# Kernel tuning notes

Hardware: AMD Instinct MI355X
Metric: run time of the kernel (lower is better)

Reference implementation:

```python
import jax, jax.numpy as jnp
import numpy as np

N = 50000      # num_nodes
NT = 300000    # unique (s, o) pairs
R = 64         # num relations
RP = 16        # latent pseudo-relations
E = 32         # emb_dim
C = 32         # num_classes
LW = 64        # latent MLP width


def setup_inputs() -> dict:
    key = jax.random.key(0)
    ks = jax.random.split(key, 12)
    inp = {
        "s_idx": jax.random.randint(ks[0], (NT,), 0, N, dtype=jnp.int32),
        "o_idx": jax.random.randint(ks[1], (NT,), 0, N, dtype=jnp.int32),
        "nhots": jax.random.uniform(ks[2], (NT, R), dtype=jnp.float32),
        "W1a": jax.random.normal(ks[3], (R, LW), dtype=jnp.float32) * 0.1,
        "b1a": jnp.zeros((LW,), jnp.float32),
        "W1b": jax.random.normal(ks[4], (LW, RP), dtype=jnp.float32) * 0.1,
        "b1b": jnp.zeros((RP,), jnp.float32),
        "W2a": jax.random.normal(ks[5], (R, LW), dtype=jnp.float32) * 0.1,
        "b2a": jnp.zeros((LW,), jnp.float32),
        "W2b": jax.random.normal(ks[6], (LW, RP), dtype=jnp.float32) * 0.1,
        "b2b": jnp.zeros((RP,), jnp.float32),
        "weights1": jax.random.normal(ks[7], (RP, N, E), dtype=jnp.float32) * 0.05,
        "weights2": jax.random.normal(ks[8], (RP, E, C), dtype=jnp.float32) * 0.05,
        "bias1": jnp.zeros((E,), jnp.float32),
        "bias2": jnp.zeros((C,), jnp.float32),
    }
    return inp


def _mlp(x, Wa, ba, Wb, bb):
    # Linear(r, lwidth) -> ReLU -> Linear(lwidth, rp)
    return jax.nn.relu(x @ Wa + ba) @ Wb + bb


def reference(s_idx, o_idx, nhots, W1a, b1a, W1b, b1b, W2a, b2a, W2b, b2b,
              weights1, weights2, bias1, bias2):
    n, rp = N, RP
    e = weights1.shape[2]
    k = jnp.arange(rp, dtype=s_idx.dtype)[:, None]   # [rp, 1]

    # hindices: rows = s (tiled k-major), cols = o * k  -> sparse (n, n*rp)
    hrows = jnp.tile(s_idx, rp)                       # [rp*nt]
    hcols = (o_idx[None, :] * k).reshape(-1)          # [rp*nt]
    # vindices: rows = s * k, cols = o (tiled)        -> sparse (n*rp, n)
    vrows = (s_idx[None, :] * k).reshape(-1)
    vcols = jnp.tile(o_idx, rp)

    # ---- layer 1: latent relation softmax + column-normalized spmm ----
    lat1 = jax.nn.softmax(_mlp(nhots, W1a, b1a, W1b, b1b), axis=1)  # [nt, rp]
    v1 = lat1.T.reshape(-1)                                          # [rp*nt], k-major
    colsum = jax.ops.segment_sum(v1, hcols, num_segments=n * rp)
    v1 = v1 / colsum[hcols]
    # spmm: out[s] += v1 * weights1.view(rp*n, e)[o*k]
    h = jax.ops.segment_sum(v1[:, None] * weights1.reshape(rp * n, e)[hcols],
                            hrows, num_segments=n)                   # [n, e]
    h = jax.nn.relu(h + bias1)

    # ---- layer 2: latent relation softmax + row-normalized spmm ----
    lat2 = jax.nn.softmax(_mlp(nhots, W2a, b2a, W2b, b2b), axis=1)   # [nt, rp]
    v2 = lat2.T.reshape(-1)
    rowsum = jax.ops.segment_sum(v2, vrows, num_segments=n * rp)
    v2 = v2 / rowsum[vrows]
    # spmm: out[s*k] += v2 * h[o]
    h2 = jax.ops.segment_sum(v2[:, None] * h[vcols],
                             vrows, num_segments=n * rp)             # [n*rp, e]
    h2 = h2.reshape(rp, n, e)

    out = jnp.einsum('rhc,rnh->nc', weights2, h2) + bias2            # [n, c]
    return out
```

## Files before the change

### kernel.cpp

```cpp
#include <hip/hip_runtime.h>
#include <hip/hip_bf16.h>

#define DEV_INLINE __device__ __forceinline__

constexpr int kN   = 50000;
constexpr int kNT  = 300000;
constexpr int kR   = 64;
constexpr int kRP  = 16;
constexpr int kE   = 32;
constexpr int kC   = 32;
constexpr int kLW  = 64;
constexpr int kNRP = kN * kRP;
constexpr int kChunks = (kN + 255) / 256;

typedef __attribute__((ext_vector_type(8))) short s8v;
typedef __attribute__((ext_vector_type(4))) float f32x4;

DEV_INLINE short f2bf(float f) {
  union { float f; unsigned u; } v; v.f = f;
  unsigned r = (v.u + 0x7fffu + ((v.u >> 16) & 1u)) >> 16;
  return (short)r;
}
DEV_INLINE float bf2f(short s) {
  union { unsigned u; float f; } v; v.u = ((unsigned)(unsigned short)s) << 16;
  return v.f;
}
DEV_INLINE float bflo(unsigned u) { union { unsigned x; float f; } a; a.x = u << 16;        return a.f; }
DEV_INLINE float bfhi(unsigned u) { union { unsigned x; float f; } a; a.x = u & 0xffff0000u; return a.f; }

union U4S8 { uint4 u; s8v s; };

DEV_INLINE void split8(const float4 A, const float4 B, s8v& hi, s8v& lo) {
  const float f[8] = {A.x, A.y, A.z, A.w, B.x, B.y, B.z, B.w};
  unsigned u[8], l[8];
#pragma unroll
  for (int i = 0; i < 8; i++) { union { float f; unsigned u; } c; c.f = f[i]; u[i] = c.u; }
#pragma unroll
  for (int i = 0; i < 8; i++) {
    union { unsigned u; float f; } t; t.u = u[i] & 0xffff0000u;
    union { float f; unsigned u; } c; c.f = f[i] - t.f; l[i] = c.u;
  }
  U4S8 H, L;
  H.u.x = (u[1] & 0xffff0000u) | (u[0] >> 16);
  H.u.y = (u[3] & 0xffff0000u) | (u[2] >> 16);
  H.u.z = (u[5] & 0xffff0000u) | (u[4] >> 16);
  H.u.w = (u[7] & 0xffff0000u) | (u[6] >> 16);
  L.u.x = (l[1] & 0xffff0000u) | (l[0] >> 16);
  L.u.y = (l[3] & 0xffff0000u) | (l[2] >> 16);
  L.u.z = (l[5] & 0xffff0000u) | (l[4] >> 16);
  L.u.w = (l[7] & 0xffff0000u) | (l[6] >> 16);
  hi = H.s; lo = L.s;
}

__global__ void __launch_bounds__(256)
k_count(const int* __restrict__ s_idx, const int* __restrict__ o_idx,
        int* __restrict__ cnt_s, int* __restrict__ cnt_o) {
  const int e = blockIdx.x * 256 + threadIdx.x;
  if (e < kNT) {
    atomicAdd(&cnt_s[s_idx[e]], 1);
    atomicAdd(&cnt_o[o_idx[e]], 1);
  }
}

__global__ void __launch_bounds__(256)
k_scan_p1(const int* __restrict__ cnt_s, const int* __restrict__ cnt_o,
          int* __restrict__ rp_s, int* __restrict__ rp_o,
          int* __restrict__ bs_s, int* __restrict__ bs_o) {
  const int b = blockIdx.x;
  const bool iso = b >= kChunks;
  const int chunk = iso ? b - kChunks : b;
  const int* cnt = iso ? cnt_o : cnt_s;
  int* rp = iso ? rp_o : rp_s;
  int* bs = iso ? bs_o : bs_s;
  __shared__ int ws[4];
  const int tid = threadIdx.x, wave = tid >> 6, lane = tid & 63;
  const int i = chunk * 256 + tid;
  int v = (i < kN) ? cnt[i] : 0;
  int incl = v;
#pragma unroll
  for (int off = 1; off < 64; off <<= 1) {
    int tmp = __shfl_up(incl, off, 64);
    if (lane >= off) incl += tmp;
  }
  if (lane == 63) ws[wave] = incl;
  __syncthreads();
  int add = 0;
#pragma unroll
  for (int w = 0; w < 4; w++) if (w < wave) add += ws[w];
  incl += add;
  if (i < kN) rp[i + 1] = incl;
  if (tid == 255) bs[chunk] = incl;
}

__global__ void __launch_bounds__(256)
k_scan_p2(int* __restrict__ bs_s, int* __restrict__ bs_o) {
  __shared__ int ws[4];
  const int tid = threadIdx.x, wave = tid >> 6, lane = tid & 63;
#pragma unroll 1
  for (int a = 0; a < 2; a++) {
    int* bs = a ? bs_o : bs_s;
    const int v = (tid < kChunks) ? bs[tid] : 0;
    int incl = v;
#pragma unroll
    for (int off = 1; off < 64; off <<= 1) {
      int tmp = __shfl_up(incl, off, 64);
      if (lane >= off) incl += tmp;
    }
    if (lane == 63) ws[wave] = incl;
    __syncthreads();
    int add = 0;
#pragma unroll
    for (int w = 0; w < 4; w++) if (w < wave) add += ws[w];
    incl += add;
    __syncthreads();
    if (tid < kChunks) bs[tid] = incl - v;
    __syncthreads();
  }
}

__global__ void __launch_bounds__(256)
k_scan_p3(const int* __restrict__ bs_s, const int* __restrict__ bs_o,
          int* __restrict__ rp_s, int* __restrict__ rp_o) {
  const int b = blockIdx.x;
  const bool iso = b >= kChunks;
  const int chunk = iso ? b - kChunks : b;
  int* rp = iso ? rp_o : rp_s;
  const int* bs = iso ? bs_o : bs_s;
  const int i = chunk * 256 + threadIdx.x;
  if (i < kN) rp[i + 1] += bs[chunk];
  if (chunk == 0 && threadIdx.x == 0) rp[0] = 0;
}

__global__ void __launch_bounds__(256)
k_scatter2(const int* __restrict__ s_idx, const int* __restrict__ o_idx,
           const int* __restrict__ rowptr_s, int* __restrict__ cursor_s,
           const int* __restrict__ rowptr_o, int* __restrict__ cursor_o,
           int2* __restrict__ eo_s, int* __restrict__ e_o) {
  const int e = blockIdx.x * 256 + threadIdx.x;
  if (e < kNT) {
    const int s = s_idx[e], o = o_idx[e];
    const int ps = atomicAdd(&cursor_s[s], 1);
    int2 v; v.x = e; v.y = o;
    eo_s[rowptr_s[s] + ps] = v;
    const int po = atomicAdd(&cursor_o[o], 1);
    e_o[rowptr_o[o] + po] = e;
  }
}

__global__ void __launch_bounds__(256)
k_wprep(const float* __restrict__ W1a, const float* __restrict__ W1b,
        const float* __restrict__ W2a, const float* __restrict__ W2b,
        short* __restrict__ Wf) {
  const int tid = threadIdx.x;
  for (int i = tid; i < 8192; i += 256) {
    const int j = i & 7, lane = (i >> 3) & 63, ks = (i >> 9) & 1,
              nt = (i >> 10) & 3, mlp = i >> 12;
    const int p = lane & 15, q8 = (lane >> 4) * 8;
    const float* Wa = mlp ? W2a : W1a;
    const float v = Wa[(ks * 32 + q8 + j) * kLW + nt * 16 + p];
    union { float f; unsigned u; } c; c.f = v;
    const short h = (short)(c.u >> 16);
    Wf[i] = h;
    Wf[8192 + i] = f2bf(v - bf2f(h));
  }
  for (int i = tid; i < 2048; i += 256) {
    const int j = i & 7, lane = (i >> 3) & 63, ks = (i >> 9) & 1, mlp = i >> 10;
    const int p = lane & 15, q8 = (lane >> 4) * 8;
    const float* Wb = mlp ? W2b : W1b;
    const float v = Wb[(ks * 32 + q8 + j) * kRP + p];
    union { float f; unsigned u; } c; c.f = v;
    const short h = (short)(c.u >> 16);
    Wf[16384 + i] = h;
    Wf[18432 + i] = f2bf(v - bf2f(h));
  }
}

__global__ void __launch_bounds__(256)
k_lat(const float* __restrict__ nhots, const short* __restrict__ Wf,
      const float* __restrict__ b1a, const float* __restrict__ b1b,
      const float* __restrict__ b2a, const float* __restrict__ b2b,
      const int* __restrict__ s_idx, const int* __restrict__ o_idx,
      float* __restrict__ lat1o, float* __restrict__ lat2o,
      float* __restrict__ C1, float* __restrict__ R2) {
  __shared__ float sHf[4][16][68];
  const int tid = threadIdx.x;
  const int wave = tid >> 6, lane = tid & 63;
  const int p = lane & 15, q = lane >> 4, q8 = (lane >> 4) * 8;

  const uint4* BaH4 = (const uint4*)(Wf);
  const uint4* BaL4 = (const uint4*)(Wf + 8192);
  const uint4* BbH4 = (const uint4*)(Wf + 16384);
  const uint4* BbL4 = (const uint4*)(Wf + 18432);

  const int w2 = (blockIdx.x * 4 + wave) * 2;

#pragma unroll 1
  for (int mlp = 0; mlp < 2; mlp++) {
    s8v Bh[4][2], Bl[4][2], Bbh[2], Bbl[2];
#pragma unroll
    for (int nt = 0; nt < 4; nt++)
#pragma unroll
      for (int ks = 0; ks < 2; ks++) {
        U4S8 a, b;
        a.u = BaH4[((mlp * 4 + nt) * 2 + ks) * 64 + lane];
        b.u = BaL4[((mlp * 4 + nt) * 2 + ks) * 64 + lane];
        Bh[nt][ks] = a.s; Bl[nt][ks] = b.s;
      }
#pragma unroll
    for (int ks = 0; ks < 2; ks++) {
      U4S8 a, b;
      a.u = BbH4[(mlp * 2 + ks) * 64 + lane];
      b.u = BbL4[(mlp * 2 + ks) * 64 + lane];
      Bbh[ks] = a.s; Bbl[ks] = b.s;
    }
    const float* bA = mlp ? b2a : b1a;
    const float* bB = mlp ? b2b : b1b;
    float bav[4];
#pragma unroll
    for (int nt = 0; nt < 4; nt++) bav[nt] = bA[nt * 16 + p];
    const float bbv = bB[p];
    float* lato = mlp ? lat2o : lat1o;
    const int* nidx = mlp ? s_idx : o_idx;
    float* part = mlp ? R2 : C1;

#pragma unroll 1
    for (int t = 0; t < 2; t++) {
      const int slot = w2 + t;
      if (slot >= kNT / 32) break;
      const int eb = slot * 32;
#pragma unroll 1
      for (int ht = 0; ht < 2; ht++) {
        const int mb = eb + ht * 16;
        int nid[4];
#pragma unroll
        for (int reg = 0; reg < 4; reg++) nid[reg] = nidx[mb + q * 4 + reg];
        const float* arow = nhots + (size_t)(mb + p) * kR;
        s8v ah[2], al[2];
#pragma unroll
        for (int ks = 0; ks < 2; ks++) {
          const float4 xa = *(const float4*)(arow + ks * 32 + q8);
          const float4 xb = *(const float4*)(arow + ks * 32 + q8 + 4);
          split8(xa, xb, ah[ks], al[ks]);
        }
        f32x4 acc[4];
#pragma unroll
        for (int nt = 0; nt < 4; nt++) {
          acc[nt] = (f32x4)0.f;
#pragma unroll
          for (int ks = 0; ks < 2; ks++) {
            acc[nt] = __builtin_amdgcn_mfma_f32_16x16x32_bf16(ah[ks], Bh[nt][ks], acc[nt], 0, 0, 0);
            acc[nt] = __builtin_amdgcn_mfma_f32_16x16x32_bf16(ah[ks], Bl[nt][ks], acc[nt], 0, 0, 0);
            acc[nt] = __builtin_amdgcn_mfma_f32_16x16x32_bf16(al[ks], Bh[nt][ks], acc[nt], 0, 0, 0);
          }
        }
#pragma unroll
        for (int nt = 0; nt < 4; nt++)
#pragma unroll
          for (int reg = 0; reg < 4; reg++)
            sHf[wave][q * 4 + reg][nt * 16 + p] = fmaxf(acc[nt][reg] + bav[nt], 0.f);
        const float* hr = &sHf[wave][p][0];
        s8v hh[2], hl[2];
#pragma unroll
        for (int ks = 0; ks < 2; ks++) {
          const float4 xa = *(const float4*)(hr + ks * 32 + q8);
          const float4 xb = *(const float4*)(hr + ks * 32 + q8 + 4);
          split8(xa, xb, hh[ks], hl[ks]);
        }
        f32x4 accB = (f32x4)0.f;
#pragma unroll
        for (int ks = 0; ks < 2; ks++) {
          accB = __builtin_amdgcn_mfma_f32_16x16x32_bf16(hh[ks], Bbh[ks], accB, 0, 0, 0);
          accB = __builtin_amdgcn_mfma_f32_16x16x32_bf16(hh[ks], Bbl[ks], accB, 0, 0, 0);
          accB = __builtin_amdgcn_mfma_f32_16x16x32_bf16(hl[ks], Bbh[ks], accB, 0, 0, 0);
        }
#pragma unroll
        for (int reg = 0; reg < 4; reg++) {
          const float v = accB[reg] + bbv;
          float m = v;
#pragma unroll
          for (int d = 1; d < 16; d <<= 1) m = fmaxf(m, __shfl_xor(m, d));
          const float e = __expf(v - m);
          float sum = e;
#pragma unroll
          for (int d = 1; d < 16; d <<= 1) sum += __shfl_xor(sum, d);
          const float lv = e / sum;
          lato[(size_t)(mb + q * 4 + reg) * kRP + p] = lv;
          atomicAdd(&part[(size_t)nid[reg] * kRP + p], lv);
        }
      }
    }
  }
}

__global__ void __launch_bounds__(256)
k_tots(const float* __restrict__ C1, const float* __restrict__ R2,
       float* __restrict__ tots) {
  __shared__ float s0[4], s1[4];
  const int tid = threadIdx.x, wave = tid >> 6, lane = tid & 63;
  float a = 0.f, b = 0.f;
  for (int i = blockIdx.x * 256 + tid; i < kN; i += gridDim.x * 256) {
    a += C1[(size_t)i * kRP];
    b += R2[(size_t)i * kRP];
  }
#pragma unroll
  for (int d = 1; d < 64; d <<= 1) { a += __shfl_xor(a, d); b += __shfl_xor(b, d); }
  if (lane == 0) { s0[wave] = a; s1[wave] = b; }
  __syncthreads();
  if (tid == 0) {
    atomicAdd(&tots[0], s0[0] + s0[1] + s0[2] + s0[3]);
    atomicAdd(&tots[1], s1[0] + s1[1] + s1[2] + s1[3]);
  }
}

__global__ void __launch_bounds__(256)
k_norms(const float* __restrict__ C1, const float* __restrict__ R2,
        const float* __restrict__ tots,
        float* __restrict__ csinv, float* __restrict__ rsinv) {
  const int m = blockIdx.x * 256 + threadIdx.x;
  if (m < kNRP) {
    float cs = (m == 0) ? tots[0] : 0.f;
    float rs = (m == 0) ? tots[1] : 0.f;
#pragma unroll
    for (int k = 1; k < kRP; k++) {
      if (m % k == 0) {
        const int q = m / k;
        if (q < kN) { cs += C1[q * kRP + k]; rs += R2[q * kRP + k]; }
      }
    }
    csinv[m] = (cs != 0.f) ? 1.f / cs : 0.f;
    rsinv[m] = (rs != 0.f) ? 1.f / rs : 0.f;
  }
}

__global__ void __launch_bounds__(256)
k_gbuild(const float* __restrict__ wt1, const float* __restrict__ csinv,
         unsigned* __restrict__ G8u) {
  __shared__ float sT[16][33];
  const int o = blockIdx.x;
  const int tid = threadIdx.x;
#pragma unroll
  for (int half = 0; half < 2; half++) {
    const int e = half * 256 + tid;
    const int k = e >> 5, c = e & 31;
    const int idx = o * k;
    sT[k][c] = csinv[idx] * wt1[(size_t)idx * kE + c];
  }
  __syncthreads();
  const int l = tid >> 2;
  const int c = l >> 1, kh = l & 1;
  const int j0 = (2 * tid) & 7;
  const int k0 = kh * 8 + j0, k1 = k0 + 1;
  const unsigned lo = (unsigned short)f2bf(sT[k0][c]);
  const unsigned hi = (unsigned short)f2bf(sT[k1][c]);
  G8u[(size_t)o * 256 + tid] = lo | (hi << 16);
}

__global__ void __launch_bounds__(256)
k_layer1g(const int* __restrict__ rowptr, const int2* __restrict__ eo,
          const float* __restrict__ lat1, const uint4* __restrict__ G8,
          const float* __restrict__ bias1, float* __restrict__ h) {
  const int tid = threadIdx.x;
  const int wave = tid >> 6, lane = tid & 63;
  const int c = lane >> 1, kh = lane & 1;
  const float b1 = bias1[c];
  for (int s = blockIdx.x * 4 + wave; s < kN; s += gridDim.x * 4) {
    float acc = 0.f;
    const int beg = rowptr[s], end = rowptr[s + 1];
    for (int j = beg; j < end; j++) {
      const int2 E = eo[j];
      const uint4 g = G8[(size_t)E.y * 64 + lane];
      const float4 la = *(const float4*)(lat1 + (size_t)E.x * kRP + kh * 8);
      const float4 lb = *(const float4*)(lat1 + (size_t)E.x * kRP + kh * 8 + 4);
      acc = fmaf(la.x, bflo(g.x), acc); acc = fmaf(la.y, bfhi(g.x), acc);
      acc = fmaf(la.z, bflo(g.y), acc); acc = fmaf(la.w, bfhi(g.y), acc);
      acc = fmaf(lb.x, bflo(g.z), acc); acc = fmaf(lb.y, bfhi(g.z), acc);
      acc = fmaf(lb.z, bflo(g.w), acc); acc = fmaf(lb.w, bfhi(g.w), acc);
    }
    acc += __shfl_xor(acc, 1);
    if (kh == 0) h[(size_t)s * kE + c] = fmaxf(acc + b1, 0.f);
  }
}

__global__ void __launch_bounds__(256)
k_u(const int* __restrict__ rowptr, const int2* __restrict__ eo,
    const float* __restrict__ lat2, const float* __restrict__ rsinv,
    const float* __restrict__ h, short* __restrict__ Ub,
    float* __restrict__ pblk) {
  __shared__ float sacc[kE];
  const int tid = threadIdx.x;
  const int wave = tid >> 6, lane = tid & 63;
  const int c = lane & 31, half = lane >> 5;
  if (tid < kE) sacc[tid] = 0.f;
  __syncthreads();
  float hpart = 0.f;
  for (int s = blockIdx.x * 4 + wave; s < kN; s += gridDim.x * 4) {
    float u[8];
#pragma unroll
    for (int kk = 0; kk < 8; kk++) u[kk] = 0.f;
    const int beg = rowptr[s], end = rowptr[s + 1];
    for (int j = beg; j < end; j++) {
      const int2 E = eo[j];
      const float hv = h[(size_t)E.y * kE + c];
      const float4* lp = (const float4*)(lat2 + (size_t)E.x * kRP) + half * 2;
      const float4 la = lp[0], lb = lp[1];
      const float lv[8] = {la.x, la.y, la.z, la.w, lb.x, lb.y, lb.z, lb.w};
#pragma unroll
      for (int kk = 0; kk < 8; kk++) u[kk] = fmaf(lv[kk], hv, u[kk]);
    }
    if (half == 0) hpart += u[0];
#pragma unroll
    for (int kk = 0; kk < 8; kk++) {
      const int k = half * 8 + kk;
      if (k >= 1)
        Ub[((size_t)s * 15 + (k - 1)) * kE + c] = f2bf(u[kk] * rsinv[s * k]);
    }
  }
  atomicAdd(&sacc[c], hpart);
  __syncthreads();
  if (tid < kE) pblk[(size_t)blockIdx.x * kE + tid] = sacc[tid];
}

__global__ void __launch_bounds__(256)
k_hred(const float* __restrict__ pblk, int nblk, float* __restrict__ hrow0) {
  __shared__ float sacc[kE];
  const int tid = threadIdx.x;
  if (tid < kE) sacc[tid] = 0.f;
  __syncthreads();
  const int total = nblk * kE;
  float r = 0.f;
  for (int i = blockIdx.x * 256 + tid; i < total; i += gridDim.x * 256)
    r += pblk[i];
  atomicAdd(&sacc[tid & 31], r);
  __syncthreads();
  if (tid < kE) atomicAdd(&hrow0[tid], sacc[tid]);
}

__global__ void __launch_bounds__(256)
k_h2(const short* __restrict__ Ub, const float* __restrict__ hrow0,
     const float* __restrict__ rsinv, short* __restrict__ H2) {
  const int tid = threadIdx.x;
  const int g = tid >> 5, c = tid & 31;
  const int n = blockIdx.x * 8 + g;
  const float rs0 = rsinv[0];
  int nm[16];
  nm[0] = 0; nm[1] = 0;
#pragma unroll
  for (int k = 2; k < kRP; k++) nm[k] = n % k;
#pragma unroll
  for (int r = 0; r < kRP; r++) {
    float row = 0.f;
    if (r == 0 && n == 0) row = hrow0[c] * rs0;
#pragma unroll
    for (int k = r + 1; k < kRP; k++) {
      const int target = (k - (r * 50000) % k) % k;
      if (nm[k] == target) {
        const int s = (r * 50000 + n) / k;
        row += bf2f(Ub[((size_t)s * 15 + (k - 1)) * kE + c]);
      }
    }
    H2[((size_t)n * kRP + r) * kE + c] = f2bf(row);
  }
}

__global__ void __launch_bounds__(256)
k_einsum(const short* __restrict__ H2, const float* __restrict__ W2,
         const float* __restrict__ bias2, float* __restrict__ out) {
  __shared__ short sBWh[16 * 2 * 64 * 8];
  __shared__ short sBWl[16 * 2 * 64 * 8];
  const int tid = threadIdx.x;
  for (int i = tid; i < 16384; i += 256) {
    const int j = i & 7, ln = (i >> 3) & 63, nt = (i >> 9) & 1, ks = i >> 10;
    const int pp = ln & 15, qq8 = (ln >> 4) * 8;
    const float v = W2[(ks * 32 + qq8 + j) * 32 + nt * 16 + pp];
    const short h = f2bf(v);
    sBWh[i] = h;
    sBWl[i] = f2bf(v - bf2f(h));
  }
  __syncthreads();
  const int wave = tid >> 6, lane = tid & 63;
  const int p = lane & 15, q = lane >> 4, q8 = q * 8;
  const float bias0 = bias2[p], bias1v = bias2[16 + p];
  for (int tile = blockIdx.x * 4 + wave; tile < kN / 16; tile += gridDim.x * 4) {
    const int mb = tile * 16;
    f32x4 acc0 = (f32x4)0.f, acc1 = (f32x4)0.f;
    const short* arow = H2 + (size_t)(mb + p) * 512 + q8;
#pragma unroll
    for (int ks = 0; ks < 16; ks++) {
      const s8v a   = *(const s8v*)(arow + ks * 32);
      const s8v b0h = *(const s8v*)(sBWh + ((ks * 2 + 0) * 64 + lane) * 8);
      const s8v b0l = *(const s8v*)(sBWl + ((ks * 2 + 0) * 64 + lane) * 8);
      const s8v b1h = *(const s8v*)(sBWh + ((ks * 2 + 1) * 64 + lane) * 8);
      const s8v b1l = *(const s8v*)(sBWl + ((ks * 2 + 1) * 64 + lane) * 8);
      acc0 = __builtin_amdgcn_mfma_f32_16x16x32_bf16(a, b0h, acc0, 0, 0, 0);
      acc0 = __builtin_amdgcn_mfma_f32_16x16x32_bf16(a, b0l, acc0, 0, 0, 0);
      acc1 = __builtin_amdgcn_mfma_f32_16x16x32_bf16(a, b1h, acc1, 0, 0, 0);
      acc1 = __builtin_amdgcn_mfma_f32_16x16x32_bf16(a, b1l, acc1, 0, 0, 0);
    }
#pragma unroll
    for (int reg = 0; reg < 4; reg++) {
      const int n = mb + q * 4 + reg;
      out[(size_t)n * kC + p]      = acc0[reg] + bias0;
      out[(size_t)n * kC + 16 + p] = acc1[reg] + bias1v;
    }
  }
}

extern "C" void kernel_launch(void* const* d_in, const int* in_sizes, int n_in,
                              void* d_out, int out_size, void* d_ws, size_t ws_size,
                              hipStream_t stream) {
  (void)in_sizes; (void)n_in; (void)out_size; (void)ws_size;
  const int* s_idx = (const int*)d_in[0];
  const int* o_idx = (const int*)d_in[1];
  const float* nhots = (const float*)d_in[2];
  const float* W1a = (const float*)d_in[3]; const float* b1a = (const float*)d_in[4];
  const float* W1b = (const float*)d_in[5]; const float* b1b = (const float*)d_in[6];
  const float* W2a = (const float*)d_in[7]; const float* b2a = (const float*)d_in[8];
  const float* W2b = (const float*)d_in[9]; const float* b2b = (const float*)d_in[10];
  const float* wt1 = (const float*)d_in[11]; const float* wt2 = (const float*)d_in[12];
  const float* bias1 = (const float*)d_in[13]; const float* bias2 = (const float*)d_in[14];

  char* ws = (char*)d_ws;
  size_t off = 0;
  auto alloc = [&](size_t bytes) -> char* {
    char* p = ws + off;
    off = (off + bytes + 255) & ~(size_t)255;
    return p;
  };
  char*  z0       = ws;
  int*   cnt_s    = (int*)  alloc((size_t)kN * 4);
  int*   cnt_o    = (int*)  alloc((size_t)kN * 4);
  int*   cursor_s = (int*)  alloc((size_t)kN * 4);
  int*   cursor_o = (int*)  alloc((size_t)kN * 4);
  float* tots     = (float*)alloc(8);
  float* hrow0    = (float*)alloc((size_t)kE * 4);
  float* C1       = (float*)alloc((size_t)kNRP * 4);
  float* R2       = (float*)alloc((size_t)kNRP * 4);
  const size_t zbytes = (size_t)((ws + off) - z0);
  short* Wf       = (short*)alloc((size_t)20480 * 2);
  int*   bs_s     = (int*)  alloc((size_t)kChunks * 4);
  int*   bs_o     = (int*)  alloc((size_t)kChunks * 4);
  int*   rowptr_s = (int*)  alloc((size_t)(kN + 1) * 4);
  int*   rowptr_o = (int*)  alloc((size_t)(kN + 1) * 4);
  float* pblk     = (float*)alloc((size_t)12500 * kE * 4);
  float* lat2     = (float*)alloc((size_t)kNT * kRP * 4);
  int2*  eo_s     = (int2*) alloc((size_t)kNT * 8);
  int*   e_o      = (int*)  alloc((size_t)kNT * 4);
  float* csinv    = (float*)alloc((size_t)kNRP * 4);
  float* rsinv    = (float*)alloc((size_t)kNRP * 4);
  float* hbuf     = (float*)alloc((size_t)kN * kE * 4);
  short* Ub       = (short*)alloc((size_t)kN * 15 * kE * 2);
  char*  Greg     = alloc((size_t)kN * 1024);
  float* lat1     = (float*)Ub;
  unsigned* G8u   = (unsigned*)Greg;
  short* H2       = (short*)Greg;

  hipMemsetAsync(z0, 0, zbytes, stream);

  const dim3 blk(256);
  const int gEdges = (kNT + 255) / 256;
  const int gLat = ((kNT / 32 + 1) / 2 + 3) / 4;

  k_count<<<gEdges, blk, 0, stream>>>(s_idx, o_idx, cnt_s, cnt_o);
  k_scan_p1<<<2 * kChunks, blk, 0, stream>>>(cnt_s, cnt_o, rowptr_s, rowptr_o, bs_s, bs_o);
  k_scan_p2<<<1, blk, 0, stream>>>(bs_s, bs_o);
  k_scan_p3<<<2 * kChunks, blk, 0, stream>>>(bs_s, bs_o, rowptr_s, rowptr_o);
  k_scatter2<<<gEdges, blk, 0, stream>>>(s_idx, o_idx, rowptr_s, cursor_s,
                                         rowptr_o, cursor_o, eo_s, e_o);
  k_wprep<<<1, blk, 0, stream>>>(W1a, W1b, W2a, W2b, Wf);
  k_lat<<<gLat, blk, 0, stream>>>(nhots, Wf, b1a, b1b, b2a, b2b,
                                  s_idx, o_idx, lat1, lat2, C1, R2);
  k_tots<<<64, blk, 0, stream>>>(C1, R2, tots);
  k_norms<<<(kNRP + 255) / 256, blk, 0, stream>>>(C1, R2, tots, csinv, rsinv);
  k_gbuild<<<kN, blk, 0, stream>>>(wt1, csinv, G8u);
  k_layer1g<<<12500, blk, 0, stream>>>(rowptr_s, eo_s, lat1, (const uint4*)G8u, bias1, hbuf);
  k_u<<<12500, blk, 0, stream>>>(rowptr_s, eo_s, lat2, rsinv, hbuf, Ub, pblk);
  k_hred<<<50, blk, 0, stream>>>(pblk, 12500, hrow0);
  k_h2<<<kN / 8, blk, 0, stream>>>(Ub, hrow0, rsinv, H2);
  k_einsum<<<782, blk, 0, stream>>>(H2, wt2, bias2, (float*)d_out);
}
```

Before: 586.3 us.

## Write latents in s-sorted CSR order, drop unused o-CSR, prefetch gather loads

```diff
diff --git a/kernel.cpp b/kernel.cpp
--- a/kernel.cpp
+++ b/kernel.cpp
@@ -53,28 +53,16 @@
 }
 
 __global__ void __launch_bounds__(256)
-k_count(const int* __restrict__ s_idx, const int* __restrict__ o_idx,
-        int* __restrict__ cnt_s, int* __restrict__ cnt_o) {
+k_count(const int* __restrict__ s_idx, int* __restrict__ cnt_s) {
   const int e = blockIdx.x * 256 + threadIdx.x;
-  if (e < kNT) {
-    atomicAdd(&cnt_s[s_idx[e]], 1);
-    atomicAdd(&cnt_o[o_idx[e]], 1);
-  }
-}
-
-__global__ void __launch_bounds__(256)
-k_scan_p1(const int* __restrict__ cnt_s, const int* __restrict__ cnt_o,
-          int* __restrict__ rp_s, int* __restrict__ rp_o,
-          int* __restrict__ bs_s, int* __restrict__ bs_o) {
-  const int b = blockIdx.x;
-  const bool iso = b >= kChunks;
-  const int chunk = iso ? b - kChunks : b;
-  const int* cnt = iso ? cnt_o : cnt_s;
-  int* rp = iso ? rp_o : rp_s;
-  int* bs = iso ? bs_o : bs_s;
+  if (e < kNT) atomicAdd(&cnt_s[s_idx[e]], 1);
+}
+
+__global__ void __launch_bounds__(256)
+k_scan_p1(const int* __restrict__ cnt, int* __restrict__ rp, int* __restrict__ bs) {
   __shared__ int ws[4];
   const int tid = threadIdx.x, wave = tid >> 6, lane = tid & 63;
-  const int i = chunk * 256 + tid;
+  const int i = blockIdx.x * 256 + tid;
   int v = (i < kN) ? cnt[i] : 0;
   int incl = v;
 #pragma unroll
@@ -89,61 +77,47 @@
   for (int w = 0; w < 4; w++) if (w < wave) add += ws[w];
   incl += add;
   if (i < kN) rp[i + 1] = incl;
-  if (tid == 255) bs[chunk] = incl;
-}
-
-__global__ void __launch_bounds__(256)
-k_scan_p2(int* __restrict__ bs_s, int* __restrict__ bs_o) {
+  if (tid == 255) bs[blockIdx.x] = incl;
+}
+
+__global__ void __launch_bounds__(256)
+k_scan_p2(int* __restrict__ bs) {
   __shared__ int ws[4];
   const int tid = threadIdx.x, wave = tid >> 6, lane = tid & 63;
-#pragma unroll 1
-  for (int a = 0; a < 2; a++) {
-    int* bs = a ? bs_o : bs_s;
-    const int v = (tid < kChunks) ? bs[tid] : 0;
-    int incl = v;
-#pragma unroll
-    for (int off = 1; off < 64; off <<= 1) {
-      int tmp = __shfl_up(incl, off, 64);
-      if (lane >= off) incl += tmp;
-    }
-    if (lane == 63) ws[wave] = incl;
-    __syncthreads();
-    int add = 0;
-#pragma unroll
-    for (int w = 0; w < 4; w++) if (w < wave) add += ws[w];
-    incl += add;
-    __syncthreads();
-    if (tid < kChunks) bs[tid] = incl - v;
-    __syncthreads();
-  }
-}
-
-__global__ void __launch_bounds__(256)
-k_scan_p3(const int* __restrict__ bs_s, const int* __restrict__ bs_o,
-          int* __restrict__ rp_s, int* __restrict__ rp_o) {
-  const int b = blockIdx.x;
-  const bool iso = b >= kChunks;
-  const int chunk = iso ? b - kChunks : b;
-  int* rp = iso ? rp_o : rp_s;
-  const int* bs = iso ? bs_o : bs_s;
-  const int i = chunk * 256 + threadIdx.x;
-  if (i < kN) rp[i + 1] += bs[chunk];
-  if (chunk == 0 && threadIdx.x == 0) rp[0] = 0;
-}
-
-__global__ void __launch_bounds__(256)
-k_scatter2(const int* __restrict__ s_idx, const int* __restrict__ o_idx,
-           const int* __restrict__ rowptr_s, int* __restrict__ cursor_s,
-           const int* __restrict__ rowptr_o, int* __restrict__ cursor_o,
-           int2* __restrict__ eo_s, int* __restrict__ e_o) {
+  const int v = (tid < kChunks) ? bs[tid] : 0;
+  int incl = v;
+#pragma unroll
+  for (int off = 1; off < 64; off <<= 1) {
+    int tmp = __shfl_up(incl, off, 64);
+    if (lane >= off) incl += tmp;
+  }
+  if (lane == 63) ws[wave] = incl;
+  __syncthreads();
+  int add = 0;
+#pragma unroll
+  for (int w = 0; w < 4; w++) if (w < wave) add += ws[w];
+  incl += add;
+  if (tid < kChunks) bs[tid] = incl - v;
+}
+
+__global__ void __launch_bounds__(256)
+k_scan_p3(const int* __restrict__ bs, int* __restrict__ rp) {
+  const int i = blockIdx.x * 256 + threadIdx.x;
+  if (i < kN) rp[i + 1] += bs[blockIdx.x];
+  if (blockIdx.x == 0 && threadIdx.x == 0) rp[0] = 0;
+}
+
+__global__ void __launch_bounds__(256)
+k_scatter(const int* __restrict__ s_idx, const int* __restrict__ o_idx,
+          const int* __restrict__ rowptr, int* __restrict__ cursor,
+          int* __restrict__ o_csr, int* __restrict__ sslot) {
   const int e = blockIdx.x * 256 + threadIdx.x;
   if (e < kNT) {
-    const int s = s_idx[e], o = o_idx[e];
-    const int ps = atomicAdd(&cursor_s[s], 1);
-    int2 v; v.x = e; v.y = o;
-    eo_s[rowptr_s[s] + ps] = v;
-    const int po = atomicAdd(&cursor_o[o], 1);
-    e_o[rowptr_o[o] + po] = e;
+    const int s = s_idx[e];
+    const int ps = atomicAdd(&cursor[s], 1);
+    const int slot = rowptr[s] + ps;
+    o_csr[slot] = o_idx[e];
+    sslot[e] = slot;
   }
 }
 
@@ -180,6 +154,7 @@
       const float* __restrict__ b1a, const float* __restrict__ b1b,
       const float* __restrict__ b2a, const float* __restrict__ b2b,
       const int* __restrict__ s_idx, const int* __restrict__ o_idx,
+      const int* __restrict__ sslot,
       float* __restrict__ lat1o, float* __restrict__ lat2o,
       float* __restrict__ C1, float* __restrict__ R2) {
   __shared__ float sHf[4][16][68];
@@ -231,9 +206,13 @@
 #pragma unroll 1
       for (int ht = 0; ht < 2; ht++) {
         const int mb = eb + ht * 16;
-        int nid[4];
-#pragma unroll
-        for (int reg = 0; reg < 4; reg++) nid[reg] = nidx[mb + q * 4 + reg];
+        int nid[4], sl[4];
+#pragma unroll
+        for (int reg = 0; reg < 4; reg++) {
+          const int m = mb + q * 4 + reg;
+          nid[reg] = nidx[m];
+          sl[reg]  = sslot[m];
+        }
         const float* arow = nhots + (size_t)(mb + p) * kR;
         s8v ah[2], al[2];
 #pragma unroll
@@ -284,7 +263,7 @@
 #pragma unroll
           for (int d = 1; d < 16; d <<= 1) sum += __shfl_xor(sum, d);
           const float lv = e / sum;
-          lato[(size_t)(mb + q * 4 + reg) * kRP + p] = lv;
+          lato[(size_t)sl[reg] * kRP + p] = lv;
           atomicAdd(&part[(size_t)nid[reg] * kRP + p], lv);
         }
       }
@@ -356,7 +335,7 @@
 }
 
 __global__ void __launch_bounds__(256)
-k_layer1g(const int* __restrict__ rowptr, const int2* __restrict__ eo,
+k_layer1g(const int* __restrict__ rowptr, const int* __restrict__ o_csr,
           const float* __restrict__ lat1, const uint4* __restrict__ G8,
           const float* __restrict__ bias1, float* __restrict__ h) {
   const int tid = threadIdx.x;
@@ -364,17 +343,33 @@
   const int c = lane >> 1, kh = lane & 1;
   const float b1 = bias1[c];
   for (int s = blockIdx.x * 4 + wave; s < kN; s += gridDim.x * 4) {
+    const int beg = rowptr[s], end = rowptr[s + 1];
     float acc = 0.f;
-    const int beg = rowptr[s], end = rowptr[s + 1];
+    int o1 = 0;
+    uint4 g0 = (uint4){0, 0, 0, 0};
+    float4 la0 = (float4){0.f, 0.f, 0.f, 0.f}, lb0 = la0;
+    if (beg < end) {
+      const int o0 = o_csr[beg];
+      if (beg + 1 < end) o1 = o_csr[beg + 1];
+      g0  = G8[(size_t)o0 * 64 + lane];
+      la0 = *(const float4*)(lat1 + (size_t)beg * kRP + kh * 8);
+      lb0 = *(const float4*)(lat1 + (size_t)beg * kRP + kh * 8 + 4);
+    }
     for (int j = beg; j < end; j++) {
-      const int2 E = eo[j];
-      const uint4 g = G8[(size_t)E.y * 64 + lane];
-      const float4 la = *(const float4*)(lat1 + (size_t)E.x * kRP + kh * 8);
-      const float4 lb = *(const float4*)(lat1 + (size_t)E.x * kRP + kh * 8 + 4);
-      acc = fmaf(la.x, bflo(g.x), acc); acc = fmaf(la.y, bfhi(g.x), acc);
-      acc = fmaf(la.z, bflo(g.y), acc); acc = fmaf(la.w, bfhi(g.y), acc);
-      acc = fmaf(lb.x, bflo(g.z), acc); acc = fmaf(lb.y, bfhi(g.z), acc);
-      acc = fmaf(lb.z, bflo(g.w), acc); acc = fmaf(lb.w, bfhi(g.w), acc);
+      int on = 0;
+      uint4 gn = (uint4){0, 0, 0, 0};
+      float4 lan = (float4){0.f, 0.f, 0.f, 0.f}, lbn = lan;
+      if (j + 2 < end) on = o_csr[j + 2];
+      if (j + 1 < end) {
+        gn  = G8[(size_t)o1 * 64 + lane];
+        lan = *(const float4*)(lat1 + (size_t)(j + 1) * kRP + kh * 8);
+        lbn = *(const float4*)(lat1 + (size_t)(j + 1) * kRP + kh * 8 + 4);
+      }
+      acc = fmaf(la0.x, bflo(g0.x), acc); acc = fmaf(la0.y, bfhi(g0.x), acc);
+      acc = fmaf(la0.z, bflo(g0.y), acc); acc = fmaf(la0.w, bfhi(g0.y), acc);
+      acc = fmaf(lb0.x, bflo(g0.z), acc); acc = fmaf(lb0.y, bfhi(g0.z), acc);
+      acc = fmaf(lb0.z, bflo(g0.w), acc); acc = fmaf(lb0.w, bfhi(g0.w), acc);
+      o1 = on; g0 = gn; la0 = lan; lb0 = lbn;
     }
     acc += __shfl_xor(acc, 1);
     if (kh == 0) h[(size_t)s * kE + c] = fmaxf(acc + b1, 0.f);
@@ -382,7 +377,7 @@
 }
 
 __global__ void __launch_bounds__(256)
-k_u(const int* __restrict__ rowptr, const int2* __restrict__ eo,
+k_u(const int* __restrict__ rowptr, const int* __restrict__ o_csr,
     const float* __restrict__ lat2, const float* __restrict__ rsinv,
     const float* __restrict__ h, short* __restrict__ Ub,
     float* __restrict__ pblk) {
@@ -398,14 +393,31 @@
 #pragma unroll
     for (int kk = 0; kk < 8; kk++) u[kk] = 0.f;
     const int beg = rowptr[s], end = rowptr[s + 1];
+    int o1 = 0;
+    float hv0 = 0.f;
+    float4 la0 = (float4){0.f, 0.f, 0.f, 0.f}, lb0 = la0;
+    if (beg < end) {
+      const int o0 = o_csr[beg];
+      if (beg + 1 < end) o1 = o_csr[beg + 1];
+      hv0 = h[(size_t)o0 * kE + c];
+      const float4* lp = (const float4*)(lat2 + (size_t)beg * kRP) + half * 2;
+      la0 = lp[0]; lb0 = lp[1];
+    }
     for (int j = beg; j < end; j++) {
-      const int2 E = eo[j];
-      const float hv = h[(size_t)E.y * kE + c];
-      const float4* lp = (const float4*)(lat2 + (size_t)E.x * kRP) + half * 2;
-      const float4 la = lp[0], lb = lp[1];
-      const float lv[8] = {la.x, la.y, la.z, la.w, lb.x, lb.y, lb.z, lb.w};
-#pragma unroll
-      for (int kk = 0; kk < 8; kk++) u[kk] = fmaf(lv[kk], hv, u[kk]);
+      int on = 0;
+      float hvn = 0.f;
+      float4 lan = (float4){0.f, 0.f, 0.f, 0.f}, lbn = lan;
+      if (j + 2 < end) on = o_csr[j + 2];
+      if (j + 1 < end) {
+        hvn = h[(size_t)o1 * kE + c];
+        const float4* lp = (const float4*)(lat2 + (size_t)(j + 1) * kRP) + half * 2;
+        lan = lp[0]; lbn = lp[1];
+      }
+      u[0] = fmaf(la0.x, hv0, u[0]); u[1] = fmaf(la0.y, hv0, u[1]);
+      u[2] = fmaf(la0.z, hv0, u[2]); u[3] = fmaf(la0.w, hv0, u[3]);
+      u[4] = fmaf(lb0.x, hv0, u[4]); u[5] = fmaf(lb0.y, hv0, u[5]);
+      u[6] = fmaf(lb0.z, hv0, u[6]); u[7] = fmaf(lb0.w, hv0, u[7]);
+      o1 = on; hv0 = hvn; la0 = lan; lb0 = lbn;
     }
     if (half == 0) hpart += u[0];
 #pragma unroll
@@ -528,9 +540,7 @@
   };
   char*  z0       = ws;
   int*   cnt_s    = (int*)  alloc((size_t)kN * 4);
-  int*   cnt_o    = (int*)  alloc((size_t)kN * 4);
   int*   cursor_s = (int*)  alloc((size_t)kN * 4);
-  int*   cursor_o = (int*)  alloc((size_t)kN * 4);
   float* tots     = (float*)alloc(8);
   float* hrow0    = (float*)alloc((size_t)kE * 4);
   float* C1       = (float*)alloc((size_t)kNRP * 4);
@@ -538,13 +548,12 @@
   const size_t zbytes = (size_t)((ws + off) - z0);
   short* Wf       = (short*)alloc((size_t)20480 * 2);
   int*   bs_s     = (int*)  alloc((size_t)kChunks * 4);
-  int*   bs_o     = (int*)  alloc((size_t)kChunks * 4);
   int*   rowptr_s = (int*)  alloc((size_t)(kN + 1) * 4);
-  int*   rowptr_o = (int*)  alloc((size_t)(kN + 1) * 4);
-  float* pblk     = (float*)alloc((size_t)12500 * kE * 4);
+  int*   pblk     = (int*)  nullptr;
+  float* pblkf    = (float*)alloc((size_t)12500 * kE * 4);
   float* lat2     = (float*)alloc((size_t)kNT * kRP * 4);
-  int2*  eo_s     = (int2*) alloc((size_t)kNT * 8);
-  int*   e_o      = (int*)  alloc((size_t)kNT * 4);
+  int*   o_csr    = (int*)  alloc((size_t)kNT * 4);
+  int*   sslot    = (int*)  alloc((size_t)kNT * 4);
   float* csinv    = (float*)alloc((size_t)kNRP * 4);
   float* rsinv    = (float*)alloc((size_t)kNRP * 4);
   float* hbuf     = (float*)alloc((size_t)kN * kE * 4);
@@ -553,6 +562,7 @@
   float* lat1     = (float*)Ub;
   unsigned* G8u   = (unsigned*)Greg;
   short* H2       = (short*)Greg;
+  (void)pblk;
 
   hipMemsetAsync(z0, 0, zbytes, stream);
 
@@ -560,21 +570,21 @@
   const int gEdges = (kNT + 255) / 256;
   const int gLat = ((kNT / 32 + 1) / 2 + 3) / 4;
 
-  k_count<<<gEdges, blk, 0, stream>>>(s_idx, o_idx, cnt_s, cnt_o);
-  k_scan_p1<<<2 * kChunks, blk, 0, stream>>>(cnt_s, cnt_o, rowptr_s, rowptr_o, bs_s, bs_o);
-  k_scan_p2<<<1, blk, 0, stream>>>(bs_s, bs_o);
-  k_scan_p3<<<2 * kChunks, blk, 0, stream>>>(bs_s, bs_o, rowptr_s, rowptr_o);
-  k_scatter2<<<gEdges, blk, 0, stream>>>(s_idx, o_idx, rowptr_s, cursor_s,
-                                         rowptr_o, cursor_o, eo_s, e_o);
+  k_count<<<gEdges, blk, 0, stream>>>(s_idx, cnt_s);
+  k_scan_p1<<<kChunks, blk, 0, stream>>>(cnt_s, rowptr_s, bs_s);
+  k_scan_p2<<<1, blk, 0, stream>>>(bs_s);
+  k_scan_p3<<<kChunks, blk, 0, stream>>>(bs_s, rowptr_s);
+  k_scatter<<<gEdges, blk, 0, stream>>>(s_idx, o_idx, rowptr_s, cursor_s,
+                                        o_csr, sslot);
   k_wprep<<<1, blk, 0, stream>>>(W1a, W1b, W2a, W2b, Wf);
   k_lat<<<gLat, blk, 0, stream>>>(nhots, Wf, b1a, b1b, b2a, b2b,
-                                  s_idx, o_idx, lat1, lat2, C1, R2);
+                                  s_idx, o_idx, sslot, lat1, lat2, C1, R2);
   k_tots<<<64, blk, 0, stream>>>(C1, R2, tots);
   k_norms<<<(kNRP + 255) / 256, blk, 0, stream>>>(C1, R2, tots, csinv, rsinv);
   k_gbuild<<<kN, blk, 0, stream>>>(wt1, csinv, G8u);
-  k_layer1g<<<12500, blk, 0, stream>>>(rowptr_s, eo_s, lat1, (const uint4*)G8u, bias1, hbuf);
-  k_u<<<12500, blk, 0, stream>>>(rowptr_s, eo_s, lat2, rsinv, hbuf, Ub, pblk);
-  k_hred<<<50, blk, 0, stream>>>(pblk, 12500, hrow0);
+  k_layer1g<<<12500, blk, 0, stream>>>(rowptr_s, o_csr, lat1, (const uint4*)G8u, bias1, hbuf);
+  k_u<<<12500, blk, 0, stream>>>(rowptr_s, o_csr, lat2, rsinv, hbuf, Ub, pblkf);
+  k_hred<<<50, blk, 0, stream>>>(pblkf, 12500, hrow0);
   k_h2<<<kN / 8, blk, 0, stream>>>(Ub, hrow0, rsinv, H2);
   k_einsum<<<782, blk, 0, stream>>>(H2, wt2, bias2, (float*)d_out);
 }
```

Result: faster. 556.2 us (-5.1%).
